# Performance work log

Hardware: AMD Instinct MI355X
Metric: run time of the kernel (lower is better)

The kernel has to match this reference:

```python
import jax, jax.numpy as jnp
import numpy as np

S, C, K = 1024, 4096, 4


def setup_inputs() -> dict:
    key = jax.random.key(0)
    ks = jax.random.split(key, 12)
    log_delta = jax.random.normal(ks[0], (), dtype=jnp.float32)
    log_tau = jax.random.normal(ks[1], (), dtype=jnp.float32)
    log_lambda = jax.random.normal(ks[2], (), dtype=jnp.float32)
    # extinction probs in (0,1)
    E = jax.random.uniform(ks[3], (S,), dtype=jnp.float32, minval=0.01, maxval=0.9)
    # log conditional clade probabilities (finite, roughly log-prob scale)
    log_Pi = jax.random.normal(ks[4], (C, S), dtype=jnp.float32) - 2.0
    s_C1 = jax.random.randint(ks[5], (S,), 0, S, dtype=jnp.int32)
    s_C2 = jax.random.randint(ks[6], (S,), 0, S, dtype=jnp.int32)
    recip = (jax.random.uniform(ks[7], (S, S)) < 0.05).astype(jnp.float32)
    recip = jnp.maximum(recip, jnp.eye(S, dtype=jnp.float32))  # every node has >=1 recipient
    splits_c1 = jax.random.randint(ks[8], (C, K), 0, C, dtype=jnp.int32)
    splits_c2 = jax.random.randint(ks[9], (C, K), 0, C, dtype=jnp.int32)
    log_q = jax.nn.log_softmax(jax.random.normal(ks[10], (C, K), dtype=jnp.float32), axis=-1)
    is_leaf = jax.random.uniform(ks[11], (C,)) < 0.25
    return {
        'log_delta': log_delta, 'log_tau': log_tau, 'log_lambda': log_lambda,
        'E': E, 'log_Pi': log_Pi, 's_C1': s_C1, 's_C2': s_C2,
        'Recipients_mat': recip, 'splits_c1': splits_c1, 'splits_c2': splits_c2,
        'log_q': log_q, 'is_leaf': is_leaf, 'root_id': 0,
    }


def reference(log_delta, log_tau, log_lambda, E, log_Pi, s_C1, s_C2,
              Recipients_mat, splits_c1, splits_c2, log_q, is_leaf, root_id):
    # rates via softplus, event probabilities
    delta = jax.nn.softplus(log_delta)
    tau = jax.nn.softplus(log_tau)
    lam = jax.nn.softplus(log_lambda)
    rs = 1.0 + delta + tau + lam
    p_S, p_D, p_T, p_L = 1.0 / rs, delta / rs, tau / rs, lam / rs

    # ---- E-step: single Jacobi update of extinction probabilities ----
    cnt = jnp.maximum(Recipients_mat.sum(axis=1), 1.0)           # [S]
    Ebar = (Recipients_mat @ E) / cnt                            # [S] mean over recipients
    E_new = p_L + p_D * E * E + p_T * E * Ebar + p_S * E[s_C1] * E[s_C2]

    # ---- Pi update in log space (Jacobi over clades x species) ----
    lpS, lpD, lpT = jnp.log(p_S), jnp.log(p_D), jnp.log(p_T)
    # log mean of Pi over transfer recipients: logTbar [C,S]
    m = jnp.max(log_Pi, axis=1, keepdims=True)                   # [C,1]
    sums = jnp.exp(log_Pi - m) @ Recipients_mat.T                # [C,S]
    logTbar = jnp.log(jnp.maximum(sums, 1e-30)) - jnp.log(cnt)[None, :] + m

    A = log_Pi[splits_c1]                                        # [C,K,S] child-clade 1
    B = log_Pi[splits_c2]                                        # [C,K,S] child-clade 2
    Af, Ag = A[:, :, s_C1], A[:, :, s_C2]                        # gather species children
    Bf, Bg = B[:, :, s_C1], B[:, :, s_C2]
    lq = log_q[:, :, None]
    # speciation: children go to the two species children (both orders)
    spec = lpS + jax.nn.logsumexp(lq + jnp.logaddexp(Af + Bg, Ag + Bf), axis=1)
    # duplication: both children stay on species s
    dup = lpD + jax.nn.logsumexp(lq + A + B, axis=1)
    # transfer: one child stays, the other goes to a recipient (averaged)
    TbA, TbB = logTbar[splits_c1], logTbar[splits_c2]            # [C,K,S]
    trans = lpT + jax.nn.logsumexp(lq + jnp.logaddexp(A + TbB, B + TbA), axis=1)
    # speciation-loss: clade follows one species child, other lineage goes extinct
    logE = jnp.log(E_new)                                        # E_new > 0 (p_L > 0)
    sl = lpS + jnp.logaddexp(log_Pi[:, s_C1] + logE[s_C2][None, :],
                             log_Pi[:, s_C2] + logE[s_C1][None, :])
    combined = jax.nn.logsumexp(jnp.stack([spec, dup, trans, sl], axis=0), axis=0)
    log_Pi_new = jnp.where(is_leaf[:, None], log_Pi, combined)

    # log-likelihood at the root clade
    return jax.nn.logsumexp(log_Pi_new[root_id])
```

## Files before the change

kernel.cpp:

```cpp
#include <hip/hip_runtime.h>
#include <math.h>

#define S 1024
#define C 4096
#define K 4
#define NSLOT 8

__device__ __forceinline__ float softplusf(float x) {
    return fmaxf(x, 0.0f) + log1pf(expf(-fabsf(x)));
}
__device__ __forceinline__ float logaddexpf_(float a, float b) {
    float mx = fmaxf(a, b), mn = fminf(a, b);
    return mx + log1pf(expf(mn - mx));
}
__device__ __forceinline__ float wave_sum64(float v) {
    for (int o = 32; o > 0; o >>= 1) v += __shfl_down(v, o, 64);
    return v;
}
__device__ __forceinline__ float wave_max64(float v) {
    for (int o = 32; o > 0; o >>= 1) v = fmaxf(v, __shfl_down(v, o, 64));
    return v;
}

__global__ __launch_bounds__(256) void k_main(
    const float* __restrict__ E, const float* __restrict__ logPi,
    const float* __restrict__ Recip,
    const int* __restrict__ sC1, const int* __restrict__ sC2,
    const int* __restrict__ sp1, const int* __restrict__ sp2,
    const int* __restrict__ rootp,
    const float* __restrict__ ld, const float* __restrict__ lt,
    const float* __restrict__ ll,
    float* __restrict__ logE, float* __restrict__ logTbar) {
    __shared__ __align__(16) float w[NSLOT][S];
    __shared__ __align__(16) float els[S];
    __shared__ float msh[NSLOT];
    int t = threadIdx.x;
    int root = rootp[0];

    for (int slot = 0; slot < NSLOT; ++slot) {
        int row = (slot < K) ? sp1[root * K + slot] : sp2[root * K + (slot - K)];
        const float* src = logPi + (size_t)row * S;
        for (int k = t; k < S; k += 256) w[slot][k] = src[k];
    }
    for (int k = t; k < S; k += 256) els[k] = E[k];
    __syncthreads();

    int wave = t >> 6, lane = t & 63;
    for (int s2 = 0; s2 < 2; ++s2) {
        int slot = wave * 2 + s2;
        float m = -INFINITY;
        for (int k = lane; k < S; k += 64) m = fmaxf(m, w[slot][k]);
        m = wave_max64(m);
        if (lane == 0) msh[slot] = m;
    }
    __syncthreads();
    for (int slot = 0; slot < NSLOT; ++slot) {
        float m = msh[slot];
        for (int k = t; k < S; k += 256) w[slot][k] = expf(w[slot][k] - m);
    }
    __syncthreads();

    int j = blockIdx.x * 4 + wave;
    const float4* rrow = (const float4*)(Recip + (size_t)j * S);
    const float4* ev4 = (const float4*)els;
    float4 aw[NSLOT];
    float4 ac = make_float4(0.f, 0.f, 0.f, 0.f);
    float4 ae = make_float4(0.f, 0.f, 0.f, 0.f);
#pragma unroll
    for (int s = 0; s < NSLOT; ++s) aw[s] = make_float4(0.f, 0.f, 0.f, 0.f);

#pragma unroll
    for (int i0 = 0; i0 < S / 4; i0 += 64) {
        int i = i0 + lane;
        float4 r = rrow[i];
        float4 e = ev4[i];
        ac.x += r.x; ac.y += r.y; ac.z += r.z; ac.w += r.w;
        ae.x += r.x * e.x; ae.y += r.y * e.y; ae.z += r.z * e.z; ae.w += r.w * e.w;
#pragma unroll
        for (int s = 0; s < NSLOT; ++s) {
            float4 wv = ((const float4*)w[s])[i];
            aw[s].x += r.x * wv.x; aw[s].y += r.y * wv.y;
            aw[s].z += r.z * wv.z; aw[s].w += r.w * wv.w;
        }
    }
    float c = wave_sum64(ac.x + ac.y + ac.z + ac.w);
    float ed = wave_sum64(ae.x + ae.y + ae.z + ae.w);
    float as[NSLOT];
#pragma unroll
    for (int s = 0; s < NSLOT; ++s)
        as[s] = wave_sum64(aw[s].x + aw[s].y + aw[s].z + aw[s].w);

    if (lane == 0) {
        float cnt = fmaxf(c, 1.0f);
        float logCnt = logf(cnt);
#pragma unroll
        for (int s = 0; s < NSLOT; ++s)
            logTbar[s * S + j] = logf(fmaxf(as[s], 1e-30f)) - logCnt + msh[s];
        float delta = softplusf(ld[0]);
        float tau = softplusf(lt[0]);
        float lam = softplusf(ll[0]);
        float rs = 1.0f + delta + tau + lam;
        float pS = 1.0f / rs, pD = delta / rs, pT = tau / rs, pL = lam / rs;
        float Ej = els[j];
        float en = pL + pD * Ej * Ej + pT * Ej * (ed / cnt)
                 + pS * els[sC1[j]] * els[sC2[j]];
        logE[j] = logf(en);
    }
}

__global__ __launch_bounds__(1024) void k_final(
    const float* __restrict__ logPi, const int* __restrict__ sC1,
    const int* __restrict__ sC2, const int* __restrict__ sp1,
    const int* __restrict__ sp2, const float* __restrict__ logq,
    const void* __restrict__ isLeaf, const int* __restrict__ rootp,
    const float* __restrict__ ld, const float* __restrict__ lt,
    const float* __restrict__ ll,
    const float* __restrict__ logE, const float* __restrict__ logTbar,
    float* __restrict__ out) {
    __shared__ float sA[NSLOT][S];
    __shared__ float sLogE[S];
    __shared__ float sRoot[S];
    __shared__ float red[1024];
    int t = threadIdx.x;
    int root = rootp[0];

    for (int slot = 0; slot < NSLOT; ++slot) {
        int row = (slot < K) ? sp1[root * K + slot] : sp2[root * K + (slot - K)];
        sA[slot][t] = logPi[(size_t)row * S + t];
    }
    sLogE[t] = logE[t];
    sRoot[t] = logPi[(size_t)root * S + t];
    __syncthreads();

    float delta = softplusf(ld[0]);
    float tau = softplusf(lt[0]);
    float lam = softplusf(ll[0]);
    float rs = 1.0f + delta + tau + lam;
    float lpS = logf(1.0f / rs), lpD = logf(delta / rs), lpT = logf(tau / rs);

    int j = t;
    int f = sC1[j], g = sC2[j];

    float vs[K], vd[K], vt[K];
    float ms = -INFINITY, md = -INFINITY, mt = -INFINITY;
#pragma unroll
    for (int k = 0; k < K; ++k) {
        float lq = logq[root * K + k];
        float Aj = sA[k][j], Bj = sA[4 + k][j];
        float Af = sA[k][f], Ag = sA[k][g];
        float Bf = sA[4 + k][f], Bg = sA[4 + k][g];
        vs[k] = lq + logaddexpf_(Af + Bg, Ag + Bf);
        vd[k] = lq + Aj + Bj;
        float TbAj = logTbar[k * S + j];
        float TbBj = logTbar[(4 + k) * S + j];
        vt[k] = lq + logaddexpf_(Aj + TbBj, Bj + TbAj);
        ms = fmaxf(ms, vs[k]); md = fmaxf(md, vd[k]); mt = fmaxf(mt, vt[k]);
    }
    float ss = 0.f, sd_ = 0.f, st = 0.f;
#pragma unroll
    for (int k = 0; k < K; ++k) {
        ss += expf(vs[k] - ms);
        sd_ += expf(vd[k] - md);
        st += expf(vt[k] - mt);
    }
    float vspec = lpS + ms + logf(ss);
    float vdup = lpD + md + logf(sd_);
    float vtrans = lpT + mt + logf(st);
    float vsl = lpS + logaddexpf_(sRoot[f] + sLogE[g], sRoot[g] + sLogE[f]);

    float cm = fmaxf(fmaxf(vspec, vdup), fmaxf(vtrans, vsl));
    float comb = cm + logf(expf(vspec - cm) + expf(vdup - cm) +
                           expf(vtrans - cm) + expf(vsl - cm));

    unsigned int u = ((const unsigned int*)isLeaf)[root];
    bool leaf = ((u & 0xFFu) != 0u) || (u == 0x3F800000u);
    float x = leaf ? sRoot[j] : comb;

    red[t] = x;
    __syncthreads();
    for (int o = 512; o > 0; o >>= 1) {
        if (t < o) red[t] = fmaxf(red[t], red[t + o]);
        __syncthreads();
    }
    float m = red[0];
    __syncthreads();
    red[t] = expf(x - m);
    __syncthreads();
    for (int o = 512; o > 0; o >>= 1) {
        if (t < o) red[t] += red[t + o];
        __syncthreads();
    }
    if (t == 0) out[0] = m + logf(red[0]);
}

extern "C" void kernel_launch(void* const* d_in, const int* in_sizes, int n_in,
                              void* d_out, int out_size, void* d_ws, size_t ws_size,
                              hipStream_t stream) {
    const float* log_delta = (const float*)d_in[0];
    const float* log_tau = (const float*)d_in[1];
    const float* log_lambda = (const float*)d_in[2];
    const float* E = (const float*)d_in[3];
    const float* log_Pi = (const float*)d_in[4];
    const int* s_C1 = (const int*)d_in[5];
    const int* s_C2 = (const int*)d_in[6];
    const float* Recip = (const float*)d_in[7];
    const int* splits_c1 = (const int*)d_in[8];
    const int* splits_c2 = (const int*)d_in[9];
    const float* log_q = (const float*)d_in[10];
    const void* is_leaf = (const void*)d_in[11];
    const int* root_id = (const int*)d_in[12];
    float* out = (float*)d_out;

    float* ws = (float*)d_ws;
    float* logE = ws;
    float* logTbar = ws + S;

    k_main<<<dim3(S / 4), dim3(256), 0, stream>>>(
        E, log_Pi, Recip, s_C1, s_C2, splits_c1, splits_c2, root_id,
        log_delta, log_tau, log_lambda, logE, logTbar);
    k_final<<<dim3(1), dim3(1024), 0, stream>>>(
        log_Pi, s_C1, s_C2, splits_c1, splits_c2, log_q, is_leaf, root_id,
        log_delta, log_tau, log_lambda, logE, logTbar, out);
}
```

Before: 122.4 us.

## Fuse final reduction into main kernel via last-block atomic counter

Merges the single-block final kernel into the main kernel. Each block fences its writes and increments a global atomic counter, and the last block to finish runs the root log-sum-exp stage with 256 threads handling four species each. This removes one kernel launch and its gap, but adds a hipMemsetAsync to reset the counter plus extra shared memory, which may lower occupancy in the main phase.

```diff
diff --git a/kernel.cpp b/kernel.cpp
--- a/kernel.cpp
+++ b/kernel.cpp
@@ -2,9 +2,9 @@
 #include <math.h>
 
 #define S 1024
-#define C 4096
 #define K 4
 #define NSLOT 8
+#define NBLK 256
 
 __device__ __forceinline__ float softplusf(float x) {
     return fmaxf(x, 0.0f) + log1pf(expf(-fabsf(x)));
@@ -22,7 +22,7 @@
     return v;
 }
 
-__global__ __launch_bounds__(256) void k_main(
+__global__ __launch_bounds__(256) void k_fused(
     const float* __restrict__ E, const float* __restrict__ logPi,
     const float* __restrict__ Recip,
     const int* __restrict__ sC1, const int* __restrict__ sC2,
@@ -30,10 +30,16 @@
     const int* __restrict__ rootp,
     const float* __restrict__ ld, const float* __restrict__ lt,
     const float* __restrict__ ll,
-    float* __restrict__ logE, float* __restrict__ logTbar) {
+    const float* __restrict__ logq, const void* __restrict__ isLeaf,
+    float* __restrict__ logE, float* __restrict__ logTbar,
+    unsigned int* __restrict__ counter, float* __restrict__ out) {
     __shared__ __align__(16) float w[NSLOT][S];
     __shared__ __align__(16) float els[S];
+    __shared__ __align__(16) float sRoot[S];
     __shared__ float msh[NSLOT];
+    __shared__ float red[256];
+    __shared__ unsigned int sIsLast;
+
     int t = threadIdx.x;
     int root = rootp[0];
 
@@ -106,30 +112,26 @@
                  + pS * els[sC1[j]] * els[sC2[j]];
         logE[j] = logf(en);
     }
-}
-
-__global__ __launch_bounds__(1024) void k_final(
-    const float* __restrict__ logPi, const int* __restrict__ sC1,
-    const int* __restrict__ sC2, const int* __restrict__ sp1,
-    const int* __restrict__ sp2, const float* __restrict__ logq,
-    const void* __restrict__ isLeaf, const int* __restrict__ rootp,
-    const float* __restrict__ ld, const float* __restrict__ lt,
-    const float* __restrict__ ll,
-    const float* __restrict__ logE, const float* __restrict__ logTbar,
-    float* __restrict__ out) {
-    __shared__ float sA[NSLOT][S];
-    __shared__ float sLogE[S];
-    __shared__ float sRoot[S];
-    __shared__ float red[1024];
-    int t = threadIdx.x;
-    int root = rootp[0];
+
+    __threadfence();
+    __syncthreads();
+    if (t == 0) {
+        unsigned int old = atomicAdd(counter, 1u);
+        sIsLast = (old == NBLK - 1) ? 1u : 0u;
+    }
+    __syncthreads();
+    if (sIsLast == 0u) return;
+    __threadfence();
 
     for (int slot = 0; slot < NSLOT; ++slot) {
         int row = (slot < K) ? sp1[root * K + slot] : sp2[root * K + (slot - K)];
-        sA[slot][t] = logPi[(size_t)row * S + t];
-    }
-    sLogE[t] = logE[t];
-    sRoot[t] = logPi[(size_t)root * S + t];
+        const float* src = logPi + (size_t)row * S;
+        for (int k = t; k < S; k += 256) w[slot][k] = src[k];
+    }
+    for (int k = t; k < S; k += 256) {
+        els[k] = logE[k];
+        sRoot[k] = logPi[(size_t)root * S + k];
+    }
     __syncthreads();
 
     float delta = softplusf(ld[0]);
@@ -138,55 +140,63 @@
     float rs = 1.0f + delta + tau + lam;
     float lpS = logf(1.0f / rs), lpD = logf(delta / rs), lpT = logf(tau / rs);
 
-    int j = t;
-    int f = sC1[j], g = sC2[j];
-
-    float vs[K], vd[K], vt[K];
-    float ms = -INFINITY, md = -INFINITY, mt = -INFINITY;
-#pragma unroll
-    for (int k = 0; k < K; ++k) {
-        float lq = logq[root * K + k];
-        float Aj = sA[k][j], Bj = sA[4 + k][j];
-        float Af = sA[k][f], Ag = sA[k][g];
-        float Bf = sA[4 + k][f], Bg = sA[4 + k][g];
-        vs[k] = lq + logaddexpf_(Af + Bg, Ag + Bf);
-        vd[k] = lq + Aj + Bj;
-        float TbAj = logTbar[k * S + j];
-        float TbBj = logTbar[(4 + k) * S + j];
-        vt[k] = lq + logaddexpf_(Aj + TbBj, Bj + TbAj);
-        ms = fmaxf(ms, vs[k]); md = fmaxf(md, vd[k]); mt = fmaxf(mt, vt[k]);
-    }
-    float ss = 0.f, sd_ = 0.f, st = 0.f;
-#pragma unroll
-    for (int k = 0; k < K; ++k) {
-        ss += expf(vs[k] - ms);
-        sd_ += expf(vd[k] - md);
-        st += expf(vt[k] - mt);
-    }
-    float vspec = lpS + ms + logf(ss);
-    float vdup = lpD + md + logf(sd_);
-    float vtrans = lpT + mt + logf(st);
-    float vsl = lpS + logaddexpf_(sRoot[f] + sLogE[g], sRoot[g] + sLogE[f]);
-
-    float cm = fmaxf(fmaxf(vspec, vdup), fmaxf(vtrans, vsl));
-    float comb = cm + logf(expf(vspec - cm) + expf(vdup - cm) +
-                           expf(vtrans - cm) + expf(vsl - cm));
-
     unsigned int u = ((const unsigned int*)isLeaf)[root];
     bool leaf = ((u & 0xFFu) != 0u) || (u == 0x3F800000u);
-    float x = leaf ? sRoot[j] : comb;
-
-    red[t] = x;
-    __syncthreads();
-    for (int o = 512; o > 0; o >>= 1) {
+
+    float xv[4];
+    float xmax = -INFINITY;
+#pragma unroll
+    for (int c4 = 0; c4 < 4; ++c4) {
+        int jj = t + c4 * 256;
+        int f = sC1[jj], g = sC2[jj];
+        float vs[K], vd[K], vt[K];
+        float ms = -INFINITY, md = -INFINITY, mt = -INFINITY;
+#pragma unroll
+        for (int k = 0; k < K; ++k) {
+            float lq = logq[root * K + k];
+            float Aj = w[k][jj], Bj = w[4 + k][jj];
+            float Af = w[k][f], Ag = w[k][g];
+            float Bf = w[4 + k][f], Bg = w[4 + k][g];
+            vs[k] = lq + logaddexpf_(Af + Bg, Ag + Bf);
+            vd[k] = lq + Aj + Bj;
+            float TbAj = logTbar[k * S + jj];
+            float TbBj = logTbar[(4 + k) * S + jj];
+            vt[k] = lq + logaddexpf_(Aj + TbBj, Bj + TbAj);
+            ms = fmaxf(ms, vs[k]); md = fmaxf(md, vd[k]); mt = fmaxf(mt, vt[k]);
+        }
+        float ss = 0.f, sd_ = 0.f, st = 0.f;
+#pragma unroll
+        for (int k = 0; k < K; ++k) {
+            ss += expf(vs[k] - ms);
+            sd_ += expf(vd[k] - md);
+            st += expf(vt[k] - mt);
+        }
+        float vspec = lpS + ms + logf(ss);
+        float vdup = lpD + md + logf(sd_);
+        float vtrans = lpT + mt + logf(st);
+        float vsl = lpS + logaddexpf_(sRoot[f] + els[g], sRoot[g] + els[f]);
+
+        float cm = fmaxf(fmaxf(vspec, vdup), fmaxf(vtrans, vsl));
+        float comb = cm + logf(expf(vspec - cm) + expf(vdup - cm) +
+                               expf(vtrans - cm) + expf(vsl - cm));
+        xv[c4] = leaf ? sRoot[jj] : comb;
+        xmax = fmaxf(xmax, xv[c4]);
+    }
+
+    red[t] = xmax;
+    __syncthreads();
+    for (int o = 128; o > 0; o >>= 1) {
         if (t < o) red[t] = fmaxf(red[t], red[t + o]);
         __syncthreads();
     }
     float m = red[0];
     __syncthreads();
-    red[t] = expf(x - m);
-    __syncthreads();
-    for (int o = 512; o > 0; o >>= 1) {
+    float sum = 0.f;
+#pragma unroll
+    for (int c4 = 0; c4 < 4; ++c4) sum += expf(xv[c4] - m);
+    red[t] = sum;
+    __syncthreads();
+    for (int o = 128; o > 0; o >>= 1) {
         if (t < o) red[t] += red[t + o];
         __syncthreads();
     }
@@ -214,11 +224,11 @@
     float* ws = (float*)d_ws;
     float* logE = ws;
     float* logTbar = ws + S;
-
-    k_main<<<dim3(S / 4), dim3(256), 0, stream>>>(
+    unsigned int* counter = (unsigned int*)(ws + 9 * S);
+
+    hipMemsetAsync(counter, 0, sizeof(unsigned int), stream);
+    k_fused<<<dim3(NBLK), dim3(256), 0, stream>>>(
         E, log_Pi, Recip, s_C1, s_C2, splits_c1, splits_c2, root_id,
-        log_delta, log_tau, log_lambda, logE, logTbar);
-    k_final<<<dim3(1), dim3(1024), 0, stream>>>(
-        log_Pi, s_C1, s_C2, splits_c1, splits_c2, log_q, is_leaf, root_id,
-        log_delta, log_tau, log_lambda, logE, logTbar, out);
-}
+        log_delta, log_tau, log_lambda, log_q, is_leaf,
+        logE, logTbar, counter, out);
+}
```

Result: slower. 143.1 us (+16.9%).

## Split row exp-normalization into separate kernel and use one block per recipient row

Applied to the files above, without the earlier changes.

Moves the per-slot max and exp normalization of the eight root split rows into a small preceding kernel that writes them to workspace, instead of every block redoing it in shared memory. The dot-product kernel then uses one 256-thread block per species row, each thread handling one float4, with a cross-wave shared-memory reduction. This removes the redundant per-block staging of 9 KB rows and exp work across 256 blocks. The cost is an extra kernel launch and a dependency through global memory.

```diff
diff --git a/kernel.cpp b/kernel.cpp
--- a/kernel.cpp
+++ b/kernel.cpp
@@ -2,7 +2,6 @@
 #include <math.h>
 
 #define S 1024
-#define C 4096
 #define K 4
 #define NSLOT 8
 
@@ -17,93 +16,76 @@
     for (int o = 32; o > 0; o >>= 1) v += __shfl_down(v, o, 64);
     return v;
 }
-__device__ __forceinline__ float wave_max64(float v) {
-    for (int o = 32; o > 0; o >>= 1) v = fmaxf(v, __shfl_down(v, o, 64));
-    return v;
-}
-
-__global__ __launch_bounds__(256) void k_main(
-    const float* __restrict__ E, const float* __restrict__ logPi,
-    const float* __restrict__ Recip,
+
+__global__ __launch_bounds__(1024) void k_wrow(
+    const float* __restrict__ logPi, const int* __restrict__ sp1,
+    const int* __restrict__ sp2, const int* __restrict__ rootp,
+    float* __restrict__ wbuf, float* __restrict__ mvals) {
+    __shared__ float sm[1024];
+    int slot = blockIdx.x;
+    int t = threadIdx.x;
+    int root = rootp[0];
+    int row = (slot < K) ? sp1[root * K + slot] : sp2[root * K + (slot - K)];
+    float v = logPi[(size_t)row * S + t];
+    sm[t] = v;
+    __syncthreads();
+    for (int o = 512; o > 0; o >>= 1) {
+        if (t < o) sm[t] = fmaxf(sm[t], sm[t + o]);
+        __syncthreads();
+    }
+    float m = sm[0];
+    wbuf[slot * S + t] = expf(v - m);
+    if (t == 0) mvals[slot] = m;
+}
+
+__global__ __launch_bounds__(256) void k_dots(
+    const float* __restrict__ Recip, const float* __restrict__ wbuf,
+    const float* __restrict__ mvals, const float* __restrict__ E,
     const int* __restrict__ sC1, const int* __restrict__ sC2,
-    const int* __restrict__ sp1, const int* __restrict__ sp2,
-    const int* __restrict__ rootp,
     const float* __restrict__ ld, const float* __restrict__ lt,
     const float* __restrict__ ll,
     float* __restrict__ logE, float* __restrict__ logTbar) {
-    __shared__ __align__(16) float w[NSLOT][S];
-    __shared__ __align__(16) float els[S];
-    __shared__ float msh[NSLOT];
+    __shared__ float sw[4][10];
+    int j = blockIdx.x;
     int t = threadIdx.x;
-    int root = rootp[0];
-
-    for (int slot = 0; slot < NSLOT; ++slot) {
-        int row = (slot < K) ? sp1[root * K + slot] : sp2[root * K + (slot - K)];
-        const float* src = logPi + (size_t)row * S;
-        for (int k = t; k < S; k += 256) w[slot][k] = src[k];
-    }
-    for (int k = t; k < S; k += 256) els[k] = E[k];
-    __syncthreads();
-
     int wave = t >> 6, lane = t & 63;
-    for (int s2 = 0; s2 < 2; ++s2) {
-        int slot = wave * 2 + s2;
-        float m = -INFINITY;
-        for (int k = lane; k < S; k += 64) m = fmaxf(m, w[slot][k]);
-        m = wave_max64(m);
-        if (lane == 0) msh[slot] = m;
-    }
-    __syncthreads();
-    for (int slot = 0; slot < NSLOT; ++slot) {
-        float m = msh[slot];
-        for (int k = t; k < S; k += 256) w[slot][k] = expf(w[slot][k] - m);
-    }
-    __syncthreads();
-
-    int j = blockIdx.x * 4 + wave;
-    const float4* rrow = (const float4*)(Recip + (size_t)j * S);
-    const float4* ev4 = (const float4*)els;
-    float4 aw[NSLOT];
-    float4 ac = make_float4(0.f, 0.f, 0.f, 0.f);
-    float4 ae = make_float4(0.f, 0.f, 0.f, 0.f);
-#pragma unroll
-    for (int s = 0; s < NSLOT; ++s) aw[s] = make_float4(0.f, 0.f, 0.f, 0.f);
-
-#pragma unroll
-    for (int i0 = 0; i0 < S / 4; i0 += 64) {
-        int i = i0 + lane;
-        float4 r = rrow[i];
-        float4 e = ev4[i];
-        ac.x += r.x; ac.y += r.y; ac.z += r.z; ac.w += r.w;
-        ae.x += r.x * e.x; ae.y += r.y * e.y; ae.z += r.z * e.z; ae.w += r.w * e.w;
-#pragma unroll
-        for (int s = 0; s < NSLOT; ++s) {
-            float4 wv = ((const float4*)w[s])[i];
-            aw[s].x += r.x * wv.x; aw[s].y += r.y * wv.y;
-            aw[s].z += r.z * wv.z; aw[s].w += r.w * wv.w;
-        }
-    }
-    float c = wave_sum64(ac.x + ac.y + ac.z + ac.w);
-    float ed = wave_sum64(ae.x + ae.y + ae.z + ae.w);
-    float as[NSLOT];
-#pragma unroll
-    for (int s = 0; s < NSLOT; ++s)
-        as[s] = wave_sum64(aw[s].x + aw[s].y + aw[s].z + aw[s].w);
-
+
+    float4 r = ((const float4*)(Recip + (size_t)j * S))[t];
+    float4 e = ((const float4*)E)[t];
+
+    float p[10];
+    p[0] = r.x + r.y + r.z + r.w;
+    p[1] = r.x * e.x + r.y * e.y + r.z * e.z + r.w * e.w;
+#pragma unroll
+    for (int s = 0; s < NSLOT; ++s) {
+        float4 wv = ((const float4*)(wbuf + s * S))[t];
+        p[2 + s] = r.x * wv.x + r.y * wv.y + r.z * wv.z + r.w * wv.w;
+    }
+#pragma unroll
+    for (int q = 0; q < 10; ++q) p[q] = wave_sum64(p[q]);
     if (lane == 0) {
+#pragma unroll
+        for (int q = 0; q < 10; ++q) sw[wave][q] = p[q];
+    }
+    __syncthreads();
+    if (t == 0) {
+        float c  = sw[0][0] + sw[1][0] + sw[2][0] + sw[3][0];
+        float ed = sw[0][1] + sw[1][1] + sw[2][1] + sw[3][1];
         float cnt = fmaxf(c, 1.0f);
         float logCnt = logf(cnt);
 #pragma unroll
-        for (int s = 0; s < NSLOT; ++s)
-            logTbar[s * S + j] = logf(fmaxf(as[s], 1e-30f)) - logCnt + msh[s];
+        for (int s = 0; s < NSLOT; ++s) {
+            float as = sw[0][2 + s] + sw[1][2 + s] + sw[2][2 + s] + sw[3][2 + s];
+            logTbar[s * S + j] = logf(fmaxf(as, 1e-30f)) - logCnt + mvals[s];
+        }
         float delta = softplusf(ld[0]);
         float tau = softplusf(lt[0]);
         float lam = softplusf(ll[0]);
         float rs = 1.0f + delta + tau + lam;
         float pS = 1.0f / rs, pD = delta / rs, pT = tau / rs, pL = lam / rs;
-        float Ej = els[j];
+        float Ej = E[j];
         float en = pL + pD * Ej * Ej + pT * Ej * (ed / cnt)
-                 + pS * els[sC1[j]] * els[sC2[j]];
+                 + pS * E[sC1[j]] * E[sC2[j]];
         logE[j] = logf(en);
     }
 }
@@ -212,11 +194,15 @@
     float* out = (float*)d_out;
 
     float* ws = (float*)d_ws;
-    float* logE = ws;
+    float* logE    = ws;
     float* logTbar = ws + S;
-
-    k_main<<<dim3(S / 4), dim3(256), 0, stream>>>(
-        E, log_Pi, Recip, s_C1, s_C2, splits_c1, splits_c2, root_id,
+    float* wbuf    = ws + 9 * S;
+    float* mvals   = ws + 17 * S;
+
+    k_wrow<<<dim3(NSLOT), dim3(1024), 0, stream>>>(
+        log_Pi, splits_c1, splits_c2, root_id, wbuf, mvals);
+    k_dots<<<dim3(S), dim3(256), 0, stream>>>(
+        Recip, wbuf, mvals, E, s_C1, s_C2,
         log_delta, log_tau, log_lambda, logE, logTbar);
     k_final<<<dim3(1), dim3(1024), 0, stream>>>(
         log_Pi, s_C1, s_C2, splits_c1, splits_c2, log_q, is_leaf, root_id,
```

New measurement: 114.1 us. -6.8%, faster.
